# Optimization experiments

Measured on AMD Instinct MI355X. Metric: run time of the kernel, lower is better.

The kernel has to match this reference:

```python
import jax, jax.numpy as jnp
import numpy as np

DIM = 256
HEADS = 8
WSZ = (2, 7, 7)
SSZ = (1, 3, 3)
EPS = 1e-5


def _rel_index(wsz):
    wt, wh, ww = wsz
    coords = np.stack(np.meshgrid(np.arange(wt), np.arange(wh), np.arange(ww), indexing='ij'))
    coords = coords.reshape(3, -1)  # (3, N)
    rel = coords[:, :, None] - coords[:, None, :]  # (3, N, N)
    rel = rel.transpose(1, 2, 0).copy()  # (N, N, 3)
    rel[:, :, 0] += wt - 1
    rel[:, :, 1] += wh - 1
    rel[:, :, 2] += ww - 1
    rel[:, :, 0] *= (2 * wh - 1) * (2 * ww - 1)
    rel[:, :, 1] *= (2 * ww - 1)
    return rel.sum(-1)  # (N, N) int


def _attn_mask_np(T, H, W, wsz, ssz):
    wt, wh, ww = wsz
    st, sh, sw = ssz
    img = np.zeros((T, H, W), np.int32)
    cnt = 0
    for t in (slice(0, -wt), slice(-wt, -st), slice(-st, None)):
        for h in (slice(0, -wh), slice(-wh, -sh), slice(-sh, None)):
            for w in (slice(0, -ww), slice(-ww, -sw), slice(-sw, None)):
                img[t, h, w] = cnt
                cnt += 1
    m = img.reshape(T // wt, wt, H // wh, wh, W // ww, ww)
    m = m.transpose(0, 2, 4, 1, 3, 5).reshape(-1, wt * wh * ww)  # (nW, N)
    diff = m[:, :, None] - m[:, None, :]
    return np.where(diff != 0, -100.0, 0.0).astype(np.float32)  # (nW, N, N)


def _ln(x, w, b):
    mu = x.mean(-1, keepdims=True)
    var = jnp.mean((x - mu) ** 2, -1, keepdims=True)
    return (x - mu) * jax.lax.rsqrt(var + EPS) * w + b


def _window_partition(x, wsz):
    B, T, H, W, C = x.shape
    wt, wh, ww = wsz
    x = x.reshape(B, T // wt, wt, H // wh, wh, W // ww, ww, C)
    x = x.transpose(0, 1, 3, 5, 2, 4, 6, 7)
    return x.reshape(-1, wt * wh * ww, C)


def _window_reverse(xw, wsz, B, T, H, W):
    wt, wh, ww = wsz
    C = xw.shape[-1]
    x = xw.reshape(B, T // wt, H // wh, W // ww, wt, wh, ww, C)
    x = x.transpose(0, 1, 4, 2, 5, 3, 6, 7)
    return x.reshape(B, T, H, W, C)


def setup_inputs() -> dict:
    key = jax.random.key(0)
    ks = jax.random.split(key, 8)
    B, T, H, W = 2, 8, 56, 56
    d = DIM
    hid = 4 * d
    rpe_rows = (2 * WSZ[0] - 1) * (2 * WSZ[1] - 1) * (2 * WSZ[2] - 1)
    s = 0.02
    return {
        'x': jax.random.normal(ks[0], (B, T, H, W, d), jnp.float32),
        'norm1_w': jnp.ones((d,), jnp.float32),
        'norm1_b': jnp.zeros((d,), jnp.float32),
        'qkv_w': jax.random.normal(ks[1], (3 * d, d), jnp.float32) * s,
        'qkv_b': jnp.zeros((3 * d,), jnp.float32),
        'proj_w': jax.random.normal(ks[2], (d, d), jnp.float32) * s,
        'proj_b': jnp.zeros((d,), jnp.float32),
        'rpe_table': jax.random.normal(ks[3], (rpe_rows, HEADS), jnp.float32) * s,
        'norm2_w': jnp.ones((d,), jnp.float32),
        'norm2_b': jnp.zeros((d,), jnp.float32),
        'fc1_w': jax.random.normal(ks[4], (hid, d), jnp.float32) * s,
        'fc1_b': jnp.zeros((hid,), jnp.float32),
        'fc2_w': jax.random.normal(ks[5], (d, hid), jnp.float32) * s,
        'fc2_b': jnp.zeros((d,), jnp.float32),
    }


def reference(x, norm1_w, norm1_b, qkv_w, qkv_b, proj_w, proj_b, rpe_table,
              norm2_w, norm2_b, fc1_w, fc1_b, fc2_w, fc2_b):
    B, T, H, W, C = x.shape
    wt, wh, ww = WSZ
    N = wt * wh * ww
    hd = C // HEADS
    scale = hd ** -0.5

    shortcut = x
    h = _ln(x, norm1_w, norm1_b)
    # shifted branch: cyclic roll + mask
    h = jnp.roll(h, (-SSZ[0], -SSZ[1], -SSZ[2]), axis=(1, 2, 3))
    mask = jnp.asarray(_attn_mask_np(T, H, W, WSZ, SSZ))  # (nW, N, N)
    nW = mask.shape[0]

    xw = _window_partition(h, WSZ)  # (B*nW, N, C)
    Bw = xw.shape[0]

    qkv = xw @ qkv_w.T + qkv_b  # (Bw, N, 3C)
    qkv = qkv.reshape(Bw, N, 3, HEADS, hd).transpose(2, 0, 3, 1, 4)
    q, k, v = qkv[0], qkv[1], qkv[2]  # (Bw, H, N, hd)

    idx = _rel_index(WSZ)  # (N, N)
    bias = rpe_table[idx].transpose(2, 0, 1)  # (heads, N, N)

    attn = jnp.einsum('bhnd,bhmd->bhnm', q * scale, k) + bias[None]
    attn = attn.reshape(B, nW, HEADS, N, N) + mask[None, :, None]
    attn = jax.nn.softmax(attn, axis=-1).reshape(Bw, HEADS, N, N)

    out = jnp.einsum('bhnm,bhmd->bhnd', attn, v)
    out = out.transpose(0, 2, 1, 3).reshape(Bw, N, C)
    out = out @ proj_w.T + proj_b

    out = _window_reverse(out, WSZ, B, T, H, W)
    out = jnp.roll(out, (SSZ[0], SSZ[1], SSZ[2]), axis=(1, 2, 3))

    x = shortcut + out
    h2 = _ln(x, norm2_w, norm2_b)
    h2 = jax.nn.gelu(h2 @ fc1_w.T + fc1_b, approximate=False)
    h2 = h2 @ fc2_w.T + fc2_b
    return x + h2
```

## Files before the change

### kernel.cpp

```cpp
#include <hip/hip_runtime.h>
#include <math.h>

#define TOKENS 50176
#define NWIN   512
#define C_DIM  256

typedef __attribute__((ext_vector_type(8))) short short8;
typedef __attribute__((ext_vector_type(4))) float f32x4;

__device__ __forceinline__ unsigned short f2bf(float f) {
    unsigned int u = __builtin_bit_cast(unsigned int, f);
    u += 0x7fffu + ((u >> 16) & 1);
    return (unsigned short)(u >> 16);
}

__device__ __forceinline__ void gll16(const void* g, void* l) {
    __builtin_amdgcn_global_load_lds(
        (const __attribute__((address_space(1))) unsigned int*)g,
        (__attribute__((address_space(3))) unsigned int*)l, 16, 0, 0);
}

__device__ __forceinline__ int win_token_to_flat(int u) {
    int g = u / 98;
    int n = u - g * 98;
    int bb  = g >> 8;
    int rem = g & 255;
    int tb = rem >> 6, hb = (rem >> 3) & 7, wb = rem & 7;
    int dt = n / 49;
    int r2 = n - dt * 49;
    int dh = r2 / 7, dw = r2 - dh * 7;
    int t = tb * 2 + dt, h = hb * 7 + dh, w = wb * 7 + dw;
    int ts = (t + 1) & 7;
    int hs = h + 3; if (hs >= 56) hs -= 56;
    int wsx = w + 3; if (wsx >= 56) wsx -= 56;
    return ((bb * 8 + ts) * 56 + hs) * 56 + wsx;
}

__global__ __launch_bounds__(256) void cvt_kernel(
        const float* __restrict__ src, unsigned short* __restrict__ dst, int n) {
    int i = blockIdx.x * 256 + threadIdx.x;
    if (i < n) dst[i] = f2bf(src[i]);
}

__global__ __launch_bounds__(256) void bm_kernel(
        const float* __restrict__ rpe, float* __restrict__ bm) {
    int i = blockIdx.x * 256 + threadIdx.x;
    int c  = i % 112;
    int t1 = i / 112;
    int r  = t1 % 112;
    int t2 = t1 / 112;
    int head = t2 & 7;
    int cls  = t2 >> 3;
    float val;
    if (c >= 98) {
        val = -1e30f;
    } else if (r >= 98) {
        val = 0.f;
    } else {
        int dt = r / 49, rr = r - dt * 49, dh = rr / 7, dw = rr - dh * 7;
        int dt2 = c / 49, cc = c - dt2 * 49, dh2 = cc / 7, dw2 = cc - dh2 * 7;
        int rt  = (cls & 4) ? (dt  == 0 ? 1 : 2) : 0;
        int rh  = (cls & 2) ? (dh  <  4 ? 1 : 2) : 0;
        int rw  = (cls & 1) ? (dw  <  4 ? 1 : 2) : 0;
        int rt2 = (cls & 4) ? (dt2 == 0 ? 1 : 2) : 0;
        int rh2 = (cls & 2) ? (dh2 <  4 ? 1 : 2) : 0;
        int rw2 = (cls & 1) ? (dw2 <  4 ? 1 : 2) : 0;
        int reg1 = rt * 9 + rh * 3 + rw, reg2 = rt2 * 9 + rh2 * 3 + rw2;
        int idx = (dt - dt2 + 1) * 169 + (dh - dh2 + 6) * 13 + (dw - dw2 + 6);
        val = rpe[idx * 8 + head] + ((reg1 == reg2) ? 0.f : -100.f);
    }
    bm[i] = val;
}

template<bool GATHER>
__global__ __launch_bounds__(256) void ln_kernel(
        const float* __restrict__ x, const float* __restrict__ w,
        const float* __restrict__ b, unsigned short* __restrict__ out) {
    int token = blockIdx.x * 4 + (threadIdx.x >> 6);
    int lane  = threadIdx.x & 63;
    size_t so = GATHER ? (size_t)win_token_to_flat(token) * C_DIM
                       : (size_t)token * C_DIM;
    const float* src = x + so;
    float v[4];
    float sum = 0.f;
#pragma unroll
    for (int j = 0; j < 4; ++j) { v[j] = src[lane + 64 * j]; sum += v[j]; }
#pragma unroll
    for (int o = 32; o > 0; o >>= 1) sum += __shfl_xor(sum, o, 64);
    float mu = sum * (1.f / 256.f);
    float var = 0.f;
#pragma unroll
    for (int j = 0; j < 4; ++j) { float d = v[j] - mu; var += d * d; }
#pragma unroll
    for (int o = 32; o > 0; o >>= 1) var += __shfl_xor(var, o, 64);
    float rstd = rsqrtf(var * (1.f / 256.f) + 1e-5f);
    unsigned short* dst = out + (size_t)token * C_DIM;
#pragma unroll
    for (int j = 0; j < 4; ++j) {
        int c = lane + 64 * j;
        dst[c] = f2bf((v[j] - mu) * rstd * w[c] + b[c]);
    }
}

template<int EPI>
__global__ __launch_bounds__(256) void mfma_gemm(
        const unsigned short* __restrict__ A, const unsigned short* __restrict__ B,
        const float* __restrict__ bias, const float* __restrict__ res,
        void* __restrict__ Cout, int M, int N, int K) {
    __shared__ __attribute__((aligned(16))) unsigned short Asm[128 * 32];
    __shared__ __attribute__((aligned(16))) unsigned short Bsm[128 * 32];
    int tid = threadIdx.x;
    int wave = tid >> 6, lane = tid & 63;
    int row0 = blockIdx.y * 128, col0 = blockIdx.x * 128;
    int wr = (wave >> 1) * 64;
    int wc = (wave & 1) * 64;

    f32x4 acc[4][4] = {};

    int sr = tid >> 2;
    int sk = (tid & 3) * 8;
    const unsigned short* Ag0 = A + (size_t)(row0 + sr) * K + sk;
    const unsigned short* Ag1 = A + (size_t)(row0 + 64 + sr) * K + sk;
    const unsigned short* Bg0 = B + (size_t)(col0 + sr) * K + sk;
    const unsigned short* Bg1 = B + (size_t)(col0 + 64 + sr) * K + sk;
    unsigned short* Al = Asm + tid * 8;
    unsigned short* Bl = Bsm + tid * 8;

    int fm = lane & 15, fk = (lane >> 4) * 8;

    for (int k0 = 0; k0 < K; k0 += 32) {
        __syncthreads();
        gll16(Ag0 + k0, Al);
        gll16(Ag1 + k0, Al + 64 * 32);
        gll16(Bg0 + k0, Bl);
        gll16(Bg1 + k0, Bl + 64 * 32);
        __syncthreads();
        short8 af[4], bf[4];
#pragma unroll
        for (int t4 = 0; t4 < 4; ++t4) {
            af[t4] = *(const short8*)&Asm[(wr + t4 * 16 + fm) * 32 + fk];
            bf[t4] = *(const short8*)&Bsm[(wc + t4 * 16 + fm) * 32 + fk];
        }
#pragma unroll
        for (int i = 0; i < 4; ++i)
#pragma unroll
            for (int j = 0; j < 4; ++j)
                acc[i][j] = __builtin_amdgcn_mfma_f32_16x16x32_bf16(
                    af[i], bf[j], acc[i][j], 0, 0, 0);
    }

    int crow0 = row0 + wr + (lane >> 4) * 4;
    int ccol0 = col0 + wc + (lane & 15);
    float bj[4];
#pragma unroll
    for (int j = 0; j < 4; ++j) bj[j] = bias[ccol0 + j * 16];

    if (EPI == 0) {
        unsigned short* C = (unsigned short*)Cout;
        float mul = (col0 < 256) ? 0.17677669529663687f : 1.f;
#pragma unroll
        for (int i = 0; i < 4; ++i)
#pragma unroll
            for (int v = 0; v < 4; ++v) {
                size_t base = (size_t)(crow0 + i * 16 + v) * N + ccol0;
#pragma unroll
                for (int j = 0; j < 4; ++j)
                    C[base + j * 16] = f2bf((acc[i][j][v] + bj[j]) * mul);
            }
    } else if (EPI == 1) {
        float* C = (float*)Cout;
#pragma unroll
        for (int i = 0; i < 4; ++i)
#pragma unroll
            for (int v = 0; v < 4; ++v) {
                int r = crow0 + i * 16 + v;
                size_t base = (size_t)win_token_to_flat(r) * C_DIM + ccol0;
#pragma unroll
                for (int j = 0; j < 4; ++j)
                    C[base + j * 16] = res[base + j * 16] + acc[i][j][v] + bj[j];
            }
    } else if (EPI == 2) {
        unsigned short* C = (unsigned short*)Cout;
#pragma unroll
        for (int i = 0; i < 4; ++i)
#pragma unroll
            for (int v = 0; v < 4; ++v) {
                size_t base = (size_t)(crow0 + i * 16 + v) * N + ccol0;
#pragma unroll
                for (int j = 0; j < 4; ++j) {
                    float val = acc[i][j][v] + bj[j];
                    C[base + j * 16] =
                        f2bf(0.5f * val * (1.f + erff(val * 0.70710678118654752f)));
                }
            }
    } else {
        float* C = (float*)Cout;
#pragma unroll
        for (int i = 0; i < 4; ++i)
#pragma unroll
            for (int v = 0; v < 4; ++v) {
                size_t base = (size_t)(crow0 + i * 16 + v) * N + ccol0;
#pragma unroll
                for (int j = 0; j < 4; ++j)
                    C[base + j * 16] = res[base + j * 16] + acc[i][j][v] + bj[j];
            }
    }
}

__global__ __launch_bounds__(256) void attn_mfma_kernel(
        const unsigned short* __restrict__ qkv, const float* __restrict__ bm,
        unsigned short* __restrict__ out) {
    __shared__ __attribute__((aligned(16))) unsigned short Vt[32][136];
    __shared__ __attribute__((aligned(16))) unsigned short Pw[4][16][136];
    int blk = blockIdx.x;
    int g = blk >> 3, head = blk & 7;
    int tid = threadIdx.x, wave = tid >> 6, lane = tid & 63;

    for (int i = tid; i < 32 * 30; i += 256) {
        int d = i / 30, c = 98 + (i - d * 30);
        Vt[d][c] = 0;
    }
    const unsigned short* vbase = qkv + (size_t)g * 98 * 768 + 512 + head * 32;
    for (int i = tid; i < 98 * 16; i += 256) {
        int n = i >> 4, dp = i & 15;
        unsigned int val = *(const unsigned int*)(vbase + (size_t)n * 768 + dp * 2);
        Vt[dp * 2][n]     = (unsigned short)val;
        Vt[dp * 2 + 1][n] = (unsigned short)(val >> 16);
    }
    {
        int m = lane >> 2, c = 112 + (lane & 3) * 4;
        *(unsigned long long*)&Pw[wave][m][c] = 0ULL;
    }
    __syncthreads();

    const unsigned short* qbase = qkv + (size_t)g * 98 * 768 + head * 32;
    const unsigned short* kbase = qbase + 256;
    int rem = g & 255;
    int cls = (((rem >> 6) == 3) << 2) | (((((rem >> 3) & 7)) == 7) << 1) | ((rem & 7) == 7);
    const float* bmh = bm + (size_t)(cls * 8 + head) * 112 * 112;

    int fm = lane & 15, fq = lane >> 4;
    int fk = fq * 8;
    unsigned short* obase = out + (size_t)g * 98 * 256 + head * 32;

    for (int s = wave; s < 7; s += 4) {
        int m0 = s * 16;
        int arow = m0 + fm; if (arow > 97) arow = 97;
        short8 af = *(const short8*)(qbase + (size_t)arow * 768 + fk);
        f32x4 S[7];
        f32x4 z = {0.f, 0.f, 0.f, 0.f};
#pragma unroll
        for (int j = 0; j < 7; ++j) {
            int krow = j * 16 + fm; if (krow > 97) krow = 97;
            short8 kf = *(const short8*)(kbase + (size_t)krow * 768 + fk);
            S[j] = __builtin_amdgcn_mfma_f32_16x16x32_bf16(af, kf, z, 0, 0, 0);
        }
        const float* bmrow = bmh + (m0 + fq * 4) * 112 + fm;
#pragma unroll
        for (int j = 0; j < 7; ++j)
#pragma unroll
            for (int v = 0; v < 4; ++v)
                S[j][v] += bmrow[v * 112 + j * 16];
        float inv[4];
#pragma unroll
        for (int v = 0; v < 4; ++v) {
            float m_ = S[0][v];
#pragma unroll
            for (int j = 1; j < 7; ++j) m_ = fmaxf(m_, S[j][v]);
#pragma unroll
            for (int o = 1; o < 16; o <<= 1) m_ = fmaxf(m_, __shfl_xor(m_, o, 64));
            float t = 0.f;
#pragma unroll
            for (int j = 0; j < 7; ++j) { S[j][v] = __expf(S[j][v] - m_); t += S[j][v]; }
#pragma unroll
            for (int o = 1; o < 16; o <<= 1) t += __shfl_xor(t, o, 64);
            inv[v] = 1.f / t;
        }
#pragma unroll
        for (int j = 0; j < 7; ++j)
#pragma unroll
            for (int v = 0; v < 4; ++v)
                Pw[wave][fq * 4 + v][j * 16 + fm] = f2bf(S[j][v]);
        f32x4 O0 = {0.f, 0.f, 0.f, 0.f}, O1 = {0.f, 0.f, 0.f, 0.f};
#pragma unroll
        for (int ks = 0; ks < 4; ++ks) {
            short8 pf = *(const short8*)&Pw[wave][fm][ks * 32 + fk];
            short8 v0 = *(const short8*)&Vt[fm][ks * 32 + fk];
            short8 v1 = *(const short8*)&Vt[16 + fm][ks * 32 + fk];
            O0 = __builtin_amdgcn_mfma_f32_16x16x32_bf16(pf, v0, O0, 0, 0, 0);
            O1 = __builtin_amdgcn_mfma_f32_16x16x32_bf16(pf, v1, O1, 0, 0, 0);
        }
#pragma unroll
        for (int v = 0; v < 4; ++v) {
            int row = m0 + fq * 4 + v;
            if (row < 98) {
                obase[(size_t)row * 256 + fm]      = f2bf(O0[v] * inv[v]);
                obase[(size_t)row * 256 + 16 + fm] = f2bf(O1[v] * inv[v]);
            }
        }
    }
}

extern "C" void kernel_launch(void* const* d_in, const int* in_sizes, int n_in,
                              void* d_out, int out_size, void* d_ws, size_t ws_size,
                              hipStream_t stream) {
    const float* x     = (const float*)d_in[0];
    const float* n1w   = (const float*)d_in[1];
    const float* n1b   = (const float*)d_in[2];
    const float* qkvw  = (const float*)d_in[3];
    const float* qkvb  = (const float*)d_in[4];
    const float* projw = (const float*)d_in[5];
    const float* projb = (const float*)d_in[6];
    const float* rpe   = (const float*)d_in[7];
    const float* n2w   = (const float*)d_in[8];
    const float* n2b   = (const float*)d_in[9];
    const float* fc1w  = (const float*)d_in[10];
    const float* fc1b  = (const float*)d_in[11];
    const float* fc2w  = (const float*)d_in[12];
    const float* fc2b  = (const float*)d_in[13];
    float* out = (float*)d_out;

    unsigned short* wqkv  = (unsigned short*)d_ws;
    unsigned short* wproj = wqkv + 768 * 256;
    unsigned short* wfc1  = wproj + 256 * 256;
    unsigned short* wfc2  = wfc1 + 1024 * 256;
    float* bm = (float*)(wfc2 + 256 * 1024);
    unsigned short* actA  = (unsigned short*)(bm + 8 * 8 * 112 * 112);
    unsigned short* attnO = actA + (size_t)TOKENS * 256;
    unsigned short* qkv_bf = attnO + (size_t)TOKENS * 256;
    unsigned short* fc1o = qkv_bf;

    bm_kernel<<<8 * 8 * 112 * 112 / 256, 256, 0, stream>>>(rpe, bm);
    cvt_kernel<<<(768 * 256 + 255) / 256, 256, 0, stream>>>(qkvw, wqkv, 768 * 256);
    cvt_kernel<<<(256 * 256 + 255) / 256, 256, 0, stream>>>(projw, wproj, 256 * 256);
    cvt_kernel<<<(1024 * 256 + 255) / 256, 256, 0, stream>>>(fc1w, wfc1, 1024 * 256);
    cvt_kernel<<<(256 * 1024 + 255) / 256, 256, 0, stream>>>(fc2w, wfc2, 256 * 1024);

    ln_kernel<true><<<TOKENS / 4, 256, 0, stream>>>(x, n1w, n1b, actA);
    mfma_gemm<0><<<dim3(768 / 128, TOKENS / 128), 256, 0, stream>>>(
        actA, wqkv, qkvb, nullptr, qkv_bf, TOKENS, 768, 256);
    attn_mfma_kernel<<<NWIN * 8, 256, 0, stream>>>(qkv_bf, bm, attnO);
    mfma_gemm<1><<<dim3(256 / 128, TOKENS / 128), 256, 0, stream>>>(
        attnO, wproj, projb, x, out, TOKENS, 256, 256);
    ln_kernel<false><<<TOKENS / 4, 256, 0, stream>>>(out, n2w, n2b, actA);
    mfma_gemm<2><<<dim3(1024 / 128, TOKENS / 128), 256, 0, stream>>>(
        actA, wfc1, fc1b, nullptr, fc1o, TOKENS, 1024, 256);
    mfma_gemm<3><<<dim3(256 / 128, TOKENS / 128), 256, 0, stream>>>(
        fc1o, wfc2, fc2b, out, out, TOKENS, 256, 1024);
}
```

Baseline: 407.7 us.

## Swizzle GEMM LDS tiles, swap MFMA operands for vector stores, add fc2 kernel

The GEMMs now XOR-swizzle their LDS tiles to cut bank conflicts. They swap the MFMA operand order so each lane holds four consecutive output columns, which enables float4 and packed-bf16 vector stores in the epilogues. Launch order becomes column-major over row tiles, so consecutive blocks reuse the same weight tile. A dedicated fc2 kernel uses 64-row by full-256-column tiles, and LayerNorm uses float4 loads and packed stores. These target LDS conflicts and uncoalesced scalar epilogue stores, at the cost of more code and a fixed grid tied to the token count.

Result: slower. 433.0 us (+6.2%).

```diff
diff --git a/kernel.cpp b/kernel.cpp
--- a/kernel.cpp
+++ b/kernel.cpp
@@ -3,10 +3,11 @@
 
 #define TOKENS 50176
 #define NWIN   512
-#define C_DIM  256
+#define MR     392
 
 typedef __attribute__((ext_vector_type(8))) short short8;
 typedef __attribute__((ext_vector_type(4))) float f32x4;
+typedef __attribute__((ext_vector_type(4))) unsigned short us4;
 
 __device__ __forceinline__ unsigned short f2bf(float f) {
     unsigned int u = __builtin_bit_cast(unsigned int, f);
@@ -78,132 +79,197 @@
         const float* __restrict__ b, unsigned short* __restrict__ out) {
     int token = blockIdx.x * 4 + (threadIdx.x >> 6);
     int lane  = threadIdx.x & 63;
-    size_t so = GATHER ? (size_t)win_token_to_flat(token) * C_DIM
-                       : (size_t)token * C_DIM;
-    const float* src = x + so;
-    float v[4];
-    float sum = 0.f;
-#pragma unroll
-    for (int j = 0; j < 4; ++j) { v[j] = src[lane + 64 * j]; sum += v[j]; }
+    size_t so = GATHER ? (size_t)win_token_to_flat(token) * 256
+                       : (size_t)token * 256;
+    float4 v = *(const float4*)(x + so + lane * 4);
+    float sum = v.x + v.y + v.z + v.w;
 #pragma unroll
     for (int o = 32; o > 0; o >>= 1) sum += __shfl_xor(sum, o, 64);
     float mu = sum * (1.f / 256.f);
-    float var = 0.f;
-#pragma unroll
-    for (int j = 0; j < 4; ++j) { float d = v[j] - mu; var += d * d; }
+    float d0 = v.x - mu, d1 = v.y - mu, d2 = v.z - mu, d3 = v.w - mu;
+    float var = d0 * d0 + d1 * d1 + d2 * d2 + d3 * d3;
 #pragma unroll
     for (int o = 32; o > 0; o >>= 1) var += __shfl_xor(var, o, 64);
     float rstd = rsqrtf(var * (1.f / 256.f) + 1e-5f);
-    unsigned short* dst = out + (size_t)token * C_DIM;
-#pragma unroll
-    for (int j = 0; j < 4; ++j) {
-        int c = lane + 64 * j;
-        dst[c] = f2bf((v[j] - mu) * rstd * w[c] + b[c]);
-    }
+    float4 gw = *(const float4*)(w + lane * 4);
+    float4 gb = *(const float4*)(b + lane * 4);
+    us4 pk = { f2bf(d0 * rstd * gw.x + gb.x), f2bf(d1 * rstd * gw.y + gb.y),
+               f2bf(d2 * rstd * gw.z + gb.z), f2bf(d3 * rstd * gw.w + gb.w) };
+    *(us4*)(out + (size_t)token * 256 + lane * 4) = pk;
 }
 
 template<int EPI>
-__global__ __launch_bounds__(256) void mfma_gemm(
+__global__ __launch_bounds__(256) void gemm_v2(
         const unsigned short* __restrict__ A, const unsigned short* __restrict__ B,
         const float* __restrict__ bias, const float* __restrict__ res,
-        void* __restrict__ Cout, int M, int N, int K) {
+        void* __restrict__ Cout, int N, int K) {
     __shared__ __attribute__((aligned(16))) unsigned short Asm[128 * 32];
     __shared__ __attribute__((aligned(16))) unsigned short Bsm[128 * 32];
     int tid = threadIdx.x;
     int wave = tid >> 6, lane = tid & 63;
-    int row0 = blockIdx.y * 128, col0 = blockIdx.x * 128;
+    int bid = blockIdx.x;
+    int row0 = (bid % MR) * 128;
+    int col0 = (bid / MR) * 128;
     int wr = (wave >> 1) * 64;
     int wc = (wave & 1) * 64;
 
     f32x4 acc[4][4] = {};
 
-    int sr = tid >> 2;
-    int sk = (tid & 3) * 8;
-    const unsigned short* Ag0 = A + (size_t)(row0 + sr) * K + sk;
-    const unsigned short* Ag1 = A + (size_t)(row0 + 64 + sr) * K + sk;
-    const unsigned short* Bg0 = B + (size_t)(col0 + sr) * K + sk;
-    const unsigned short* Bg1 = B + (size_t)(col0 + 64 + sr) * K + sk;
-    unsigned short* Al = Asm + tid * 8;
-    unsigned short* Bl = Bsm + tid * 8;
-
-    int fm = lane & 15, fk = (lane >> 4) * 8;
+    int srow = tid >> 2;
+    int sc = (tid & 3) ^ ((srow >> 1) & 3);
+    const unsigned short* Ag0 = A + (size_t)(row0 + srow) * K + sc * 8;
+    const unsigned short* Ag1 = A + (size_t)(row0 + 64 + srow) * K + sc * 8;
+    const unsigned short* Bg0 = B + (size_t)(col0 + srow) * K + sc * 8;
+    const unsigned short* Bg1 = B + (size_t)(col0 + 64 + srow) * K + sc * 8;
+    unsigned short* Al0 = Asm + tid * 8;
+    unsigned short* Al1 = Asm + (256 + tid) * 8;
+    unsigned short* Bl0 = Bsm + tid * 8;
+    unsigned short* Bl1 = Bsm + (256 + tid) * 8;
+
+    int fm = lane & 15, fq = lane >> 4;
 
     for (int k0 = 0; k0 < K; k0 += 32) {
         __syncthreads();
-        gll16(Ag0 + k0, Al);
-        gll16(Ag1 + k0, Al + 64 * 32);
-        gll16(Bg0 + k0, Bl);
-        gll16(Bg1 + k0, Bl + 64 * 32);
+        gll16(Ag0 + k0, Al0);
+        gll16(Ag1 + k0, Al1);
+        gll16(Bg0 + k0, Bl0);
+        gll16(Bg1 + k0, Bl1);
         __syncthreads();
-        short8 af[4], bf[4];
-#pragma unroll
-        for (int t4 = 0; t4 < 4; ++t4) {
-            af[t4] = *(const short8*)&Asm[(wr + t4 * 16 + fm) * 32 + fk];
-            bf[t4] = *(const short8*)&Bsm[(wc + t4 * 16 + fm) * 32 + fk];
-        }
+        short8 tf[4], wf[4];
+#pragma unroll
+        for (int mt = 0; mt < 4; ++mt) {
+            int r = wr + mt * 16 + fm;
+            tf[mt] = *(const short8*)&Asm[(r * 4 + (fq ^ ((r >> 1) & 3))) * 8];
+        }
+#pragma unroll
+        for (int nt = 0; nt < 4; ++nt) {
+            int r = wc + nt * 16 + fm;
+            wf[nt] = *(const short8*)&Bsm[(r * 4 + (fq ^ ((r >> 1) & 3))) * 8];
+        }
+#pragma unroll
+        for (int mt = 0; mt < 4; ++mt)
+#pragma unroll
+            for (int nt = 0; nt < 4; ++nt)
+                acc[mt][nt] = __builtin_amdgcn_mfma_f32_16x16x32_bf16(
+                    wf[nt], tf[mt], acc[mt][nt], 0, 0, 0);
+    }
+
+    int token0 = row0 + wr + fm;
+    int wcol0  = col0 + wc + fq * 4;
+    float4 bs[4];
+#pragma unroll
+    for (int nt = 0; nt < 4; ++nt)
+        bs[nt] = *(const float4*)&bias[wcol0 + nt * 16];
+
+#pragma unroll
+    for (int mt = 0; mt < 4; ++mt) {
+        int token = token0 + mt * 16;
+        if (EPI == 1) {
+            float* C = (float*)Cout;
+            size_t tbase = (size_t)win_token_to_flat(token) * 256;
+#pragma unroll
+            for (int nt = 0; nt < 4; ++nt) {
+                size_t off = tbase + wcol0 + nt * 16;
+                float4 r4 = *(const float4*)&res[off];
+                float4 o4 = { r4.x + acc[mt][nt][0] + bs[nt].x,
+                              r4.y + acc[mt][nt][1] + bs[nt].y,
+                              r4.z + acc[mt][nt][2] + bs[nt].z,
+                              r4.w + acc[mt][nt][3] + bs[nt].w };
+                *(float4*)&C[off] = o4;
+            }
+        } else {
+            unsigned short* C = (unsigned short*)Cout;
+            size_t tbase = (size_t)token * N;
+#pragma unroll
+            for (int nt = 0; nt < 4; ++nt) {
+                float v0 = acc[mt][nt][0] + bs[nt].x;
+                float v1 = acc[mt][nt][1] + bs[nt].y;
+                float v2 = acc[mt][nt][2] + bs[nt].z;
+                float v3 = acc[mt][nt][3] + bs[nt].w;
+                if (EPI == 0) {
+                    float mul = (wcol0 + nt * 16 < 256) ? 0.17677669529663687f : 1.f;
+                    v0 *= mul; v1 *= mul; v2 *= mul; v3 *= mul;
+                } else {
+                    v0 = 0.5f * v0 * (1.f + erff(v0 * 0.70710678118654752f));
+                    v1 = 0.5f * v1 * (1.f + erff(v1 * 0.70710678118654752f));
+                    v2 = 0.5f * v2 * (1.f + erff(v2 * 0.70710678118654752f));
+                    v3 = 0.5f * v3 * (1.f + erff(v3 * 0.70710678118654752f));
+                }
+                us4 pk = { f2bf(v0), f2bf(v1), f2bf(v2), f2bf(v3) };
+                *(us4*)&C[tbase + wcol0 + nt * 16] = pk;
+            }
+        }
+    }
+}
+
+__global__ __launch_bounds__(256) void fc2_kernel(
+        const unsigned short* __restrict__ A, const unsigned short* __restrict__ W,
+        const float* __restrict__ bias, const float* __restrict__ res,
+        float* __restrict__ out) {
+    __shared__ __attribute__((aligned(16))) unsigned short As[64 * 32];
+    __shared__ __attribute__((aligned(16))) unsigned short Bs[256 * 32];
+    int tid = threadIdx.x, wave = tid >> 6, lane = tid & 63;
+    int fm = lane & 15, fq = lane >> 4;
+    int row0 = blockIdx.x * 64;
+
+    f32x4 acc[4][4] = {};
+
+    int srow = tid >> 2;
+    int sca = (tid & 3) ^ ((srow >> 1) & 3);
+    const unsigned short* Asrc = A + (size_t)(row0 + srow) * 1024 + sca * 8;
+    const unsigned short* Bsrc[4];
+#pragma unroll
+    for (int i = 0; i < 4; ++i) {
+        int s = i * 256 + tid;
+        int br = s >> 2;
+        int c = (s & 3) ^ ((br >> 1) & 3);
+        Bsrc[i] = W + (size_t)br * 1024 + c * 8;
+    }
+
+    for (int k0 = 0; k0 < 1024; k0 += 32) {
+        __syncthreads();
+        gll16(Asrc + k0, As + tid * 8);
 #pragma unroll
         for (int i = 0; i < 4; ++i)
-#pragma unroll
-            for (int j = 0; j < 4; ++j)
-                acc[i][j] = __builtin_amdgcn_mfma_f32_16x16x32_bf16(
-                    af[i], bf[j], acc[i][j], 0, 0, 0);
-    }
-
-    int crow0 = row0 + wr + (lane >> 4) * 4;
-    int ccol0 = col0 + wc + (lane & 15);
-    float bj[4];
-#pragma unroll
-    for (int j = 0; j < 4; ++j) bj[j] = bias[ccol0 + j * 16];
-
-    if (EPI == 0) {
-        unsigned short* C = (unsigned short*)Cout;
-        float mul = (col0 < 256) ? 0.17677669529663687f : 1.f;
-#pragma unroll
-        for (int i = 0; i < 4; ++i)
-#pragma unroll
-            for (int v = 0; v < 4; ++v) {
-                size_t base = (size_t)(crow0 + i * 16 + v) * N + ccol0;
-#pragma unroll
-                for (int j = 0; j < 4; ++j)
-                    C[base + j * 16] = f2bf((acc[i][j][v] + bj[j]) * mul);
-            }
-    } else if (EPI == 1) {
-        float* C = (float*)Cout;
-#pragma unroll
-        for (int i = 0; i < 4; ++i)
-#pragma unroll
-            for (int v = 0; v < 4; ++v) {
-                int r = crow0 + i * 16 + v;
-                size_t base = (size_t)win_token_to_flat(r) * C_DIM + ccol0;
-#pragma unroll
-                for (int j = 0; j < 4; ++j)
-                    C[base + j * 16] = res[base + j * 16] + acc[i][j][v] + bj[j];
-            }
-    } else if (EPI == 2) {
-        unsigned short* C = (unsigned short*)Cout;
-#pragma unroll
-        for (int i = 0; i < 4; ++i)
-#pragma unroll
-            for (int v = 0; v < 4; ++v) {
-                size_t base = (size_t)(crow0 + i * 16 + v) * N + ccol0;
-#pragma unroll
-                for (int j = 0; j < 4; ++j) {
-                    float val = acc[i][j][v] + bj[j];
-                    C[base + j * 16] =
-                        f2bf(0.5f * val * (1.f + erff(val * 0.70710678118654752f)));
-                }
-            }
-    } else {
-        float* C = (float*)Cout;
-#pragma unroll
-        for (int i = 0; i < 4; ++i)
-#pragma unroll
-            for (int v = 0; v < 4; ++v) {
-                size_t base = (size_t)(crow0 + i * 16 + v) * N + ccol0;
-#pragma unroll
-                for (int j = 0; j < 4; ++j)
-                    C[base + j * 16] = res[base + j * 16] + acc[i][j][v] + bj[j];
-            }
+            gll16(Bsrc[i] + k0, Bs + (i * 256 + tid) * 8);
+        __syncthreads();
+        short8 tf[4], wf[4];
+#pragma unroll
+        for (int mt = 0; mt < 4; ++mt) {
+            int r = mt * 16 + fm;
+            tf[mt] = *(const short8*)&As[(r * 4 + (fq ^ ((r >> 1) & 3))) * 8];
+        }
+#pragma unroll
+        for (int nt = 0; nt < 4; ++nt) {
+            int r = wave * 64 + nt * 16 + fm;
+            wf[nt] = *(const short8*)&Bs[(r * 4 + (fq ^ ((r >> 1) & 3))) * 8];
+        }
+#pragma unroll
+        for (int mt = 0; mt < 4; ++mt)
+#pragma unroll
+            for (int nt = 0; nt < 4; ++nt)
+                acc[mt][nt] = __builtin_amdgcn_mfma_f32_16x16x32_bf16(
+                    wf[nt], tf[mt], acc[mt][nt], 0, 0, 0);
+    }
+
+    int wcol0 = wave * 64 + fq * 4;
+    float4 bs[4];
+#pragma unroll
+    for (int nt = 0; nt < 4; ++nt)
+        bs[nt] = *(const float4*)&bias[wcol0 + nt * 16];
+#pragma unroll
+    for (int mt = 0; mt < 4; ++mt) {
+        size_t tbase = (size_t)(row0 + mt * 16 + fm) * 256;
+#pragma unroll
+        for (int nt = 0; nt < 4; ++nt) {
+            size_t off = tbase + wcol0 + nt * 16;
+            float4 r4 = *(const float4*)&res[off];
+            float4 o4 = { r4.x + acc[mt][nt][0] + bs[nt].x,
+                          r4.y + acc[mt][nt][1] + bs[nt].y,
+                          r4.z + acc[mt][nt][2] + bs[nt].z,
+                          r4.w + acc[mt][nt][3] + bs[nt].w };
+            *(float4*)&out[off] = o4;
+        }
     }
 }
 
@@ -337,14 +403,10 @@
     cvt_kernel<<<(256 * 1024 + 255) / 256, 256, 0, stream>>>(fc2w, wfc2, 256 * 1024);
 
     ln_kernel<true><<<TOKENS / 4, 256, 0, stream>>>(x, n1w, n1b, actA);
-    mfma_gemm<0><<<dim3(768 / 128, TOKENS / 128), 256, 0, stream>>>(
-        actA, wqkv, qkvb, nullptr, qkv_bf, TOKENS, 768, 256);
+    gemm_v2<0><<<MR * 6, 256, 0, stream>>>(actA, wqkv, qkvb, nullptr, qkv_bf, 768, 256);
     attn_mfma_kernel<<<NWIN * 8, 256, 0, stream>>>(qkv_bf, bm, attnO);
-    mfma_gemm<1><<<dim3(256 / 128, TOKENS / 128), 256, 0, stream>>>(
-        attnO, wproj, projb, x, out, TOKENS, 256, 256);
+    gemm_v2<1><<<MR * 2, 256, 0, stream>>>(attnO, wproj, projb, x, out, 256, 256);
     ln_kernel<false><<<TOKENS / 4, 256, 0, stream>>>(out, n2w, n2b, actA);
-    mfma_gemm<2><<<dim3(1024 / 128, TOKENS / 128), 256, 0, stream>>>(
-        actA, wfc1, fc1b, nullptr, fc1o, TOKENS, 1024, 256);
-    mfma_gemm<3><<<dim3(256 / 128, TOKENS / 128), 256, 0, stream>>>(
-        fc1o, wfc2, fc2b, out, out, TOKENS, 256, 1024);
-}
+    gemm_v2<2><<<MR * 8, 256, 0, stream>>>(actA, wfc1, fc1b, nullptr, fc1o, 1024, 256);
+    fc2_kernel<<<TOKENS / 64, 256, 0, stream>>>(fc1o, wfc2, fc2b, out, out);
+}
```
